# Performance work log

Measured on AMD Instinct MI355X. Metric: run time of the kernel, lower is better.

The kernel has to match this reference:

```python
import jax, jax.numpy as jnp
import numpy as np

GC = 32      # group_chans = dim // 4
DIM = 128
HEADS = 8
HD = 16      # head_dim
WS = 7       # window_size
EPS = 1e-5   # torch GroupNorm default eps


def setup_inputs() -> dict:
    key = jax.random.key(0)
    ks = jax.random.split(key, 16)
    f = lambda i, shape, s=0.1: jax.random.normal(ks[i], shape, jnp.float32) * s
    inp = {"x": jax.random.normal(ks[0], (2, 128, 56, 56, 56), jnp.float32)}
    kernels = [3, 5, 7, 9]
    names = ["loc", "s", "m", "l"]
    for j, (n, k) in enumerate(zip(names, kernels)):
        inp[f"w_{n}"] = f(1 + 2 * j, (GC, 1, k))   # depthwise conv weight
        inp[f"b_{n}"] = f(2 + 2 * j, (GC,))
    for n in ["d", "h", "w", "n"]:
        inp[f"g_{n}"] = jnp.ones((DIM,), jnp.float32)
        inp[f"bt_{n}"] = jnp.zeros((DIM,), jnp.float32)
    inp["wq"] = f(10, (DIM,))
    inp["wk"] = f(11, (DIM,))
    inp["wv"] = f(12, (DIM,))
    return inp


def dwconv1d(x, w, b):
    # x: (B, C, L), w: (C, 1, k) depthwise, SAME padding k//2
    k = w.shape[-1]
    y = jax.lax.conv_general_dilated(
        x, w, (1,), [(k // 2, k // 2)],
        dimension_numbers=("NCH", "OIH", "NCH"),
        feature_group_count=x.shape[1])
    return y + b[None, :, None]


def groupnorm(x, gamma, beta, groups):
    B, C = x.shape[0], x.shape[1]
    xg = x.reshape(B, groups, -1)
    mu = xg.mean(-1, keepdims=True)
    var = xg.var(-1, keepdims=True)
    xn = ((xg - mu) * jax.lax.rsqrt(var + EPS)).reshape(x.shape)
    bs = (1, C) + (1,) * (x.ndim - 2)
    return xn * gamma.reshape(bs) + beta.reshape(bs)


def axis_gate(s, w_loc, b_loc, w_s, b_s, w_m, b_m, w_l, b_l, g, bt):
    # s: (B, C, L) pooled signal; 4 depthwise conv branches over channel groups
    parts = [dwconv1d(s[:, i * GC:(i + 1) * GC], w, b)
             for i, (w, b) in enumerate([(w_loc, b_loc), (w_s, b_s), (w_m, b_m), (w_l, b_l)])]
    return jax.nn.sigmoid(groupnorm(jnp.concatenate(parts, axis=1), g, bt, 4))


def reference(x, w_loc, b_loc, w_s, b_s, w_m, b_m, w_l, b_l,
              g_d, bt_d, g_h, bt_h, g_w, bt_w, g_n, bt_n, wq, wk, wv):
    b, c, d, h, w = x.shape
    # axis-pooled signals
    x_d = x.mean(axis=(3, 4))  # (B,C,D)
    x_h = x.mean(axis=(2, 4))  # (B,C,H)
    x_w = x.mean(axis=(2, 3))  # (B,C,W)
    dw = (w_loc, b_loc, w_s, b_s, w_m, b_m, w_l, b_l)
    gd = axis_gate(x_d, *dw, g_d, bt_d)[:, :, :, None, None]
    gh = axis_gate(x_h, *dw, g_h, bt_h)[:, :, None, :, None]
    gw = axis_gate(x_w, *dw, g_w, bt_w)[:, :, None, None, :]
    xg = x * gd * gh * gw
    # avg-pool downsample by window_size
    dd, hh, ww = d // WS, h // WS, w // WS
    y = xg.reshape(b, c, dd, WS, hh, WS, ww, WS).mean(axis=(3, 5, 7))
    y = groupnorm(y, g_n, bt_n, 1)
    sh = (1, c, 1, 1, 1)
    # 1x1 grouped (depthwise) convs == per-channel scale, no bias
    q = (y * wq.reshape(sh)).reshape(b, HEADS, HD, -1)
    k = (y * wk.reshape(sh)).reshape(b, HEADS, HD, -1)
    v = (y * wv.reshape(sh)).reshape(b, HEADS, HD, -1)
    # channel-attention: (head_dim x head_dim) scores per head
    attn = jax.nn.softmax(jnp.einsum('bnis,bnjs->bnij', q, k) * (HD ** -0.5), axis=-1)
    o = jnp.einsum('bnij,bnjs->bnis', attn, v)      # (B, heads, hd, S)
    ca = jax.nn.sigmoid(o.mean(axis=-1).reshape(b, c, 1, 1, 1))
    return ca * xg
```

## Files before the change

### kernel.cpp

```cpp
#include <hip/hip_runtime.h>
#include <math.h>

#define B 2
#define C 128
#define DSZ 56
#define SL 3136
#define VOL 175616
#define S512 512
#define EPS 1e-5f

#define OFF_POOL 0
#define OFF_GATE 43008
#define OFF_Y    86016
#define OFF_STAT 217088
#define OFF_CA   217092
#define PCL 14336

__global__ __launch_bounds__(1024) void k1_pool(const float* __restrict__ x,
                                                float* __restrict__ ws) {
    int c = blockIdx.x, b = blockIdx.y;
    int bc = b * C + c;
    const float4* base = (const float4*)(x + (size_t)bc * VOL);
    int t = threadIdx.x;
    __shared__ float s_red[56 * 16];
    __shared__ float s_h[56];
    __shared__ float s_w[56];
    if (t < 56) { s_h[t] = 0.f; s_w[t] = 0.f; }
    bool active = (t < 784);
    int h = t / 14, w4 = t % 14;
    int lane = t & 63, wave = t >> 6;
    float hacc = 0.f, wa0 = 0.f, wa1 = 0.f, wa2 = 0.f, wa3 = 0.f;
    float4 v = active ? base[t] : make_float4(0.f, 0.f, 0.f, 0.f);
    for (int d = 0; d < 56; ++d) {
        float4 vn = make_float4(0.f, 0.f, 0.f, 0.f);
        if (d < 55 && active) vn = base[(d + 1) * 784 + t];
        float s4 = v.x + v.y + v.z + v.w;
        hacc += s4; wa0 += v.x; wa1 += v.y; wa2 += v.z; wa3 += v.w;
        float red = s4;
        #pragma unroll
        for (int off = 1; off < 64; off <<= 1) red += __shfl_xor(red, off);
        if (lane == 0) s_red[d * 16 + wave] = red;
        v = vn;
    }
    __syncthreads();
    if (active) {
        atomicAdd(&s_h[h], hacc);
        atomicAdd(&s_w[w4 * 4 + 0], wa0);
        atomicAdd(&s_w[w4 * 4 + 1], wa1);
        atomicAdd(&s_w[w4 * 4 + 2], wa2);
        atomicAdd(&s_w[w4 * 4 + 3], wa3);
    }
    __syncthreads();
    if (t < 56) {
        float dsum = 0.f;
        #pragma unroll
        for (int wv = 0; wv < 16; ++wv) dsum += s_red[t * 16 + wv];
        const float inv = 1.0f / 3136.0f;
        ws[OFF_POOL + 0 * PCL + bc * 56 + t] = dsum * inv;
        ws[OFF_POOL + 1 * PCL + bc * 56 + t] = s_h[t] * inv;
        ws[OFF_POOL + 2 * PCL + bc * 56 + t] = s_w[t] * inv;
    }
}

__global__ __launch_bounds__(256) void k2_gate(
    const float* __restrict__ w0, const float* __restrict__ b0,
    const float* __restrict__ w1, const float* __restrict__ b1,
    const float* __restrict__ w2, const float* __restrict__ b2,
    const float* __restrict__ w3, const float* __restrict__ b3,
    const float* __restrict__ g0, const float* __restrict__ be0,
    const float* __restrict__ g1, const float* __restrict__ be1,
    const float* __restrict__ g2, const float* __restrict__ be2,
    float* __restrict__ ws) {
    int idx = blockIdx.x;
    int sg = idx >> 3, rem = idx & 7;
    int b = rem >> 2, g = rem & 3;
    const float* wconv[4] = {w0, w1, w2, w3};
    const float* bconv[4] = {b0, b1, b2, b3};
    const float* gam[3] = {g0, g1, g2};
    const float* bet[3] = {be0, be1, be2};
    const int ksz[4] = {3, 5, 7, 9};
    int kg = ksz[g];
    int half = kg >> 1;
    __shared__ float s_in[32 * 56];
    __shared__ float s_wt[32 * 9];
    __shared__ float s_b[32];
    __shared__ float s_redu[8];
    int t = threadIdx.x;
    const float* sp = ws + OFF_POOL + sg * PCL + (b * C + g * 32) * 56;
    for (int e = t; e < 1792; e += 256) s_in[e] = sp[e];
    for (int e = t; e < 32 * kg; e += 256) s_wt[e] = wconv[g][e];
    if (t < 32) s_b[t] = bconv[g][t];
    __syncthreads();
    float vals[7];
    float sum = 0.f, sq = 0.f;
    {
        int ii = 0;
        for (int e = t; e < 1792; e += 256, ++ii) {
            int cl = e / 56, l = e % 56;
            float acc = s_b[cl];
            for (int tt = 0; tt < kg; ++tt) {
                int ll = l + tt - half;
                if (ll >= 0 && ll < 56) acc += s_in[cl * 56 + ll] * s_wt[cl * kg + tt];
            }
            vals[ii] = acc;
            sum += acc; sq += acc * acc;
        }
    }
    #pragma unroll
    for (int off = 1; off < 64; off <<= 1) {
        sum += __shfl_xor(sum, off);
        sq += __shfl_xor(sq, off);
    }
    int lane = t & 63, wv = t >> 6;
    if (lane == 0) { s_redu[wv] = sum; s_redu[4 + wv] = sq; }
    __syncthreads();
    sum = s_redu[0] + s_redu[1] + s_redu[2] + s_redu[3];
    sq = s_redu[4] + s_redu[5] + s_redu[6] + s_redu[7];
    float mean = sum / 1792.0f;
    float var = sq / 1792.0f - mean * mean;
    float rs = rsqrtf(var + EPS);
    float* gp = ws + OFF_GATE + sg * PCL + (b * C + g * 32) * 56;
    const float* ga = gam[sg];
    const float* be = bet[sg];
    {
        int ii = 0;
        for (int e = t; e < 1792; e += 256, ++ii) {
            int cl = e / 56;
            int cch = g * 32 + cl;
            float xn = (vals[ii] - mean) * rs * ga[cch] + be[cch];
            gp[e] = 1.0f / (1.0f + expf(-xn));
        }
    }
}

__global__ __launch_bounds__(256) void k3_pooly(const float* __restrict__ x,
                                                float* __restrict__ ws) {
    int dd = blockIdx.x, c = blockIdx.y, b = blockIdx.z;
    int bc = b * C + c;
    __shared__ float xs[SL];
    __shared__ float s_gh[56];
    __shared__ float s_gw[56];
    int t = threadIdx.x;
    const float* gp = ws + OFF_GATE;
    if (t < 56) s_gh[t] = gp[1 * PCL + bc * 56 + t];
    else if (t < 112) s_gw[t - 56] = gp[2 * PCL + bc * 56 + (t - 56)];
    float acc = 0.f;
    const float* xp = x + (size_t)bc * VOL + (size_t)dd * 7 * SL;
    int hh = (t & 63) >> 3, ww = t & 7;
    for (int dz = 0; dz < 7; ++dz) {
        __syncthreads();
        const float4* src = (const float4*)(xp + dz * SL);
        float4* dst = (float4*)xs;
        for (int e = t; e < 784; e += 256) dst[e] = src[e];
        __syncthreads();
        if (t < 64) {
            float part = 0.f;
            for (int r = 0; r < 7; ++r) {
                int h_ = hh * 7 + r;
                const float* row = &xs[h_ * 56 + ww * 7];
                float rsum = 0.f;
                #pragma unroll
                for (int q = 0; q < 7; ++q) rsum += row[q] * s_gw[ww * 7 + q];
                part += s_gh[h_] * rsum;
            }
            acc += part * gp[0 * PCL + bc * 56 + dd * 7 + dz];
        }
    }
    if (t < 64) ws[OFF_Y + bc * S512 + dd * 64 + t] = acc * (1.0f / 343.0f);
}

__global__ __launch_bounds__(256) void k4a_stats(float* __restrict__ ws) {
    int b = blockIdx.x;
    const float4* yp = (const float4*)(ws + OFF_Y + b * 65536);
    int t = threadIdx.x;
    float sum = 0.f, sq = 0.f;
    for (int e = t; e < 16384; e += 256) {
        float4 v = yp[e];
        sum += v.x + v.y + v.z + v.w;
        sq += v.x * v.x + v.y * v.y + v.z * v.z + v.w * v.w;
    }
    __shared__ float s_redu[8];
    #pragma unroll
    for (int off = 1; off < 64; off <<= 1) {
        sum += __shfl_xor(sum, off);
        sq += __shfl_xor(sq, off);
    }
    int lane = t & 63, wv = t >> 6;
    if (lane == 0) { s_redu[wv] = sum; s_redu[4 + wv] = sq; }
    __syncthreads();
    if (t == 0) {
        sum = s_redu[0] + s_redu[1] + s_redu[2] + s_redu[3];
        sq = s_redu[4] + s_redu[5] + s_redu[6] + s_redu[7];
        float mean = sum / 65536.0f;
        float var = sq / 65536.0f - mean * mean;
        ws[OFF_STAT + b * 2] = mean;
        ws[OFF_STAT + b * 2 + 1] = rsqrtf(var + EPS);
    }
}

__global__ __launch_bounds__(256) void k4b_attn(
    const float* __restrict__ gn, const float* __restrict__ btn,
    const float* __restrict__ wq, const float* __restrict__ wk,
    const float* __restrict__ wv, float* __restrict__ ws) {
    int blk = blockIdx.x;
    int b = blk >> 3, hd = blk & 7;
    __shared__ float yn[16 * 514];
    __shared__ float s_sc[256];
    __shared__ float s_ybar[16];
    int t = threadIdx.x;
    float mean = ws[OFF_STAT + b * 2];
    float rs = ws[OFF_STAT + b * 2 + 1];
    const float* yp = ws + OFF_Y + b * 65536 + hd * 16 * S512;
    for (int e = t; e < 8192; e += 256) {
        int i = e >> 9, s = e & 511;
        int cch = hd * 16 + i;
        yn[i * 514 + s] = (yp[e] - mean) * rs * gn[cch] + btn[cch];
    }
    __syncthreads();
    int i = t >> 4, j = t & 15;
    const float* ri = &yn[i * 514];
    const float* rj = &yn[j * 514];
    float g = 0.f;
    for (int s = 0; s < 512; ++s) g += ri[s] * rj[s];
    s_sc[t] = wq[hd * 16 + i] * wk[hd * 16 + j] * 0.25f * g;
    if (t < 16) {
        const float* r = &yn[t * 514];
        float sb = 0.f;
        for (int s = 0; s < 512; ++s) sb += r[s];
        s_ybar[t] = sb * (1.0f / 512.0f);
    }
    __syncthreads();
    if (t < 16) {
        float m = -1e30f;
        #pragma unroll
        for (int jj = 0; jj < 16; ++jj) m = fmaxf(m, s_sc[t * 16 + jj]);
        float den = 0.f, num = 0.f;
        #pragma unroll
        for (int jj = 0; jj < 16; ++jj) {
            float e = expf(s_sc[t * 16 + jj] - m);
            den += e;
            num += e * wv[hd * 16 + jj] * s_ybar[jj];
        }
        float o = num / den;
        ws[OFF_CA + b * C + hd * 16 + t] = 1.0f / (1.0f + expf(-o));
    }
}

__global__ __launch_bounds__(256) void k5_out(const float* __restrict__ x,
                                              const float* __restrict__ ws,
                                              float* __restrict__ out) {
    int d = blockIdx.x, c = blockIdx.y, b = blockIdx.z;
    int bc = b * C + c;
    __shared__ float s_gh[56];
    __shared__ float s_gw[56];
    int t = threadIdx.x;
    const float* gp = ws + OFF_GATE;
    if (t < 56) s_gh[t] = gp[1 * PCL + bc * 56 + t];
    else if (t < 112) s_gw[t - 56] = gp[2 * PCL + bc * 56 + (t - 56)];
    __syncthreads();
    float f = ws[OFF_CA + bc] * gp[0 * PCL + bc * 56 + d];
    const float4* xp = (const float4*)(x + (size_t)bc * VOL + (size_t)d * SL);
    float4* op = (float4*)(out + (size_t)bc * VOL + (size_t)d * SL);
    for (int e = t; e < 784; e += 256) {
        float4 v = xp[e];
        int o = e * 4;
        int h_ = o / 56;
        int w0 = o % 56;
        float fh = f * s_gh[h_];
        v.x *= fh * s_gw[w0];
        v.y *= fh * s_gw[w0 + 1];
        v.z *= fh * s_gw[w0 + 2];
        v.w *= fh * s_gw[w0 + 3];
        op[e] = v;
    }
}

extern "C" void kernel_launch(void* const* d_in, const int* in_sizes, int n_in,
                              void* d_out, int out_size, void* d_ws, size_t ws_size,
                              hipStream_t stream) {
    const float* x = (const float*)d_in[0];
    float* ws = (float*)d_ws;
    float* out = (float*)d_out;

    k1_pool<<<dim3(C, B), 1024, 0, stream>>>(x, ws);
    k2_gate<<<24, 256, 0, stream>>>(
        (const float*)d_in[1], (const float*)d_in[2],
        (const float*)d_in[3], (const float*)d_in[4],
        (const float*)d_in[5], (const float*)d_in[6],
        (const float*)d_in[7], (const float*)d_in[8],
        (const float*)d_in[9], (const float*)d_in[10],
        (const float*)d_in[11], (const float*)d_in[12],
        (const float*)d_in[13], (const float*)d_in[14],
        ws);
    k3_pooly<<<dim3(8, C, B), 256, 0, stream>>>(x, ws);
    k4a_stats<<<2, 256, 0, stream>>>(ws);
    k4b_attn<<<16, 256, 0, stream>>>(
        (const float*)d_in[15], (const float*)d_in[16],
        (const float*)d_in[17], (const float*)d_in[18],
        (const float*)d_in[19], ws);
    k5_out<<<dim3(56, C, B), 256, 0, stream>>>(x, ws, out);
}
```

Measured before the change: 443.3 us.

## Split pooling across depth slabs, widen stats reduction, vectorize attention and output

The first pooling kernel changes from one 1024-thread block per channel, which streamed all 56 depth slices, to 8 blocks per channel that each cover 7 depth slices. Partial H/W sums go to a new workspace area and a new combine kernel adds them up. The stats kernel moves to 1024 threads, the attention Gram loop reads float4 with padded rows, and the output kernel handles 4 depth slices per block with float4 W gates. The main aim is more parallelism for the memory-bound pooling pass, at the cost of an extra launch and extra workspace traffic.

```diff
diff --git a/kernel.cpp b/kernel.cpp
--- a/kernel.cpp
+++ b/kernel.cpp
@@ -3,63 +3,92 @@
 
 #define B 2
 #define C 128
-#define DSZ 56
 #define SL 3136
 #define VOL 175616
 #define S512 512
 #define EPS 1e-5f
+#define PCL 14336
 
 #define OFF_POOL 0
-#define OFF_GATE 43008
-#define OFF_Y    86016
-#define OFF_STAT 217088
-#define OFF_CA   217092
-#define PCL 14336
-
-__global__ __launch_bounds__(1024) void k1_pool(const float* __restrict__ x,
-                                                float* __restrict__ ws) {
-    int c = blockIdx.x, b = blockIdx.y;
+#define OFF_PPH  43008
+#define OFF_PPW  157696
+#define OFF_GATE 272384
+#define OFF_Y    315392
+#define OFF_STAT 446464
+#define OFF_CA   446468
+
+#define F4SUM(v) ((v).x + (v).y + (v).z + (v).w)
+
+__global__ __launch_bounds__(256) void k1_pool(const float* __restrict__ x,
+                                               float* __restrict__ ws) {
+    int dd = blockIdx.x, c = blockIdx.y, b = blockIdx.z;
     int bc = b * C + c;
-    const float4* base = (const float4*)(x + (size_t)bc * VOL);
-    int t = threadIdx.x;
-    __shared__ float s_red[56 * 16];
+    const float4* base = (const float4*)(x + (size_t)bc * VOL) + dd * 7 * 784;
+    int t = threadIdx.x;
+    int lane = t & 63, wave = t >> 6;
     __shared__ float s_h[56];
     __shared__ float s_w[56];
+    __shared__ float s_dred[7 * 4];
     if (t < 56) { s_h[t] = 0.f; s_w[t] = 0.f; }
-    bool active = (t < 784);
-    int h = t / 14, w4 = t % 14;
-    int lane = t & 63, wave = t >> 6;
-    float hacc = 0.f, wa0 = 0.f, wa1 = 0.f, wa2 = 0.f, wa3 = 0.f;
-    float4 v = active ? base[t] : make_float4(0.f, 0.f, 0.f, 0.f);
-    for (int d = 0; d < 56; ++d) {
-        float4 vn = make_float4(0.f, 0.f, 0.f, 0.f);
-        if (d < 55 && active) vn = base[(d + 1) * 784 + t];
-        float s4 = v.x + v.y + v.z + v.w;
-        hacc += s4; wa0 += v.x; wa1 += v.y; wa2 += v.z; wa3 += v.w;
-        float red = s4;
-        #pragma unroll
-        for (int off = 1; off < 64; off <<= 1) red += __shfl_xor(red, off);
-        if (lane == 0) s_red[d * 16 + wave] = red;
-        v = vn;
-    }
-    __syncthreads();
-    if (active) {
-        atomicAdd(&s_h[h], hacc);
-        atomicAdd(&s_w[w4 * 4 + 0], wa0);
-        atomicAdd(&s_w[w4 * 4 + 1], wa1);
-        atomicAdd(&s_w[w4 * 4 + 2], wa2);
-        atomicAdd(&s_w[w4 * 4 + 3], wa3);
-    }
-    __syncthreads();
+    __syncthreads();
+    float4 a0 = make_float4(0,0,0,0), a1 = make_float4(0,0,0,0);
+    float4 a2 = make_float4(0,0,0,0), a3 = make_float4(0,0,0,0);
+    #pragma unroll
+    for (int dz = 0; dz < 7; ++dz) {
+        const float4* sp = base + dz * 784;
+        float4 v0 = sp[t];
+        float4 v1 = sp[t + 256];
+        float4 v2 = sp[t + 512];
+        float4 v3 = make_float4(0,0,0,0);
+        if (t < 16) v3 = sp[t + 768];
+        a0.x += v0.x; a0.y += v0.y; a0.z += v0.z; a0.w += v0.w;
+        a1.x += v1.x; a1.y += v1.y; a1.z += v1.z; a1.w += v1.w;
+        a2.x += v2.x; a2.y += v2.y; a2.z += v2.z; a2.w += v2.w;
+        a3.x += v3.x; a3.y += v3.y; a3.z += v3.z; a3.w += v3.w;
+        float s4 = F4SUM(v0) + F4SUM(v1) + F4SUM(v2) + F4SUM(v3);
+        #pragma unroll
+        for (int off = 1; off < 64; off <<= 1) s4 += __shfl_xor(s4, off);
+        if (lane == 0) s_dred[dz * 4 + wave] = s4;
+    }
+    {
+        int s0 = t, s1 = t + 256, s2 = t + 512;
+        atomicAdd(&s_h[s0 / 14], F4SUM(a0));
+        atomicAdd(&s_h[s1 / 14], F4SUM(a1));
+        atomicAdd(&s_h[s2 / 14], F4SUM(a2));
+        int w0 = (s0 % 14) * 4, w1 = (s1 % 14) * 4, w2 = (s2 % 14) * 4;
+        atomicAdd(&s_w[w0 + 0], a0.x); atomicAdd(&s_w[w0 + 1], a0.y);
+        atomicAdd(&s_w[w0 + 2], a0.z); atomicAdd(&s_w[w0 + 3], a0.w);
+        atomicAdd(&s_w[w1 + 0], a1.x); atomicAdd(&s_w[w1 + 1], a1.y);
+        atomicAdd(&s_w[w1 + 2], a1.z); atomicAdd(&s_w[w1 + 3], a1.w);
+        atomicAdd(&s_w[w2 + 0], a2.x); atomicAdd(&s_w[w2 + 1], a2.y);
+        atomicAdd(&s_w[w2 + 2], a2.z); atomicAdd(&s_w[w2 + 3], a2.w);
+        if (t < 16) {
+            int s3 = t + 768, w3 = (s3 % 14) * 4;
+            atomicAdd(&s_h[s3 / 14], F4SUM(a3));
+            atomicAdd(&s_w[w3 + 0], a3.x); atomicAdd(&s_w[w3 + 1], a3.y);
+            atomicAdd(&s_w[w3 + 2], a3.z); atomicAdd(&s_w[w3 + 3], a3.w);
+        }
+    }
+    __syncthreads();
+    if (t < 7) {
+        float ds = s_dred[t * 4] + s_dred[t * 4 + 1] + s_dred[t * 4 + 2] + s_dred[t * 4 + 3];
+        ws[OFF_POOL + bc * 56 + dd * 7 + t] = ds * (1.0f / 3136.0f);
+    }
     if (t < 56) {
-        float dsum = 0.f;
-        #pragma unroll
-        for (int wv = 0; wv < 16; ++wv) dsum += s_red[t * 16 + wv];
-        const float inv = 1.0f / 3136.0f;
-        ws[OFF_POOL + 0 * PCL + bc * 56 + t] = dsum * inv;
-        ws[OFF_POOL + 1 * PCL + bc * 56 + t] = s_h[t] * inv;
-        ws[OFF_POOL + 2 * PCL + bc * 56 + t] = s_w[t] * inv;
-    }
+        ws[OFF_PPH + (bc * 8 + dd) * 56 + t] = s_h[t];
+        ws[OFF_PPW + (bc * 8 + dd) * 56 + t] = s_w[t];
+    }
+}
+
+__global__ __launch_bounds__(256) void k1b_combine(float* __restrict__ ws) {
+    int idx = blockIdx.x * 256 + threadIdx.x;
+    int axis = idx / 14336, rem = idx % 14336;
+    int bc = rem / 56, pos = rem % 56;
+    const float* p = ws + (axis ? OFF_PPW : OFF_PPH) + bc * 8 * 56 + pos;
+    float s = 0.f;
+    #pragma unroll
+    for (int dd = 0; dd < 8; ++dd) s += p[dd * 56];
+    ws[OFF_POOL + (1 + axis) * PCL + bc * 56 + pos] = s * (1.0f / 3136.0f);
 }
 
 __global__ __launch_bounds__(256) void k2_gate(
@@ -111,8 +140,8 @@
         sum += __shfl_xor(sum, off);
         sq += __shfl_xor(sq, off);
     }
-    int lane = t & 63, wv = t >> 6;
-    if (lane == 0) { s_redu[wv] = sum; s_redu[4 + wv] = sq; }
+    int lane = t & 63, wv_ = t >> 6;
+    if (lane == 0) { s_redu[wv_] = sum; s_redu[4 + wv_] = sq; }
     __syncthreads();
     sum = s_redu[0] + s_redu[1] + s_redu[2] + s_redu[3];
     sq = s_redu[4] + s_redu[5] + s_redu[6] + s_redu[7];
@@ -134,7 +163,7 @@
 }
 
 __global__ __launch_bounds__(256) void k3_pooly(const float* __restrict__ x,
-                                                float* __restrict__ ws) {
+                                               float* __restrict__ ws) {
     int dd = blockIdx.x, c = blockIdx.y, b = blockIdx.z;
     int bc = b * C + c;
     __shared__ float xs[SL];
@@ -169,28 +198,30 @@
     if (t < 64) ws[OFF_Y + bc * S512 + dd * 64 + t] = acc * (1.0f / 343.0f);
 }
 
-__global__ __launch_bounds__(256) void k4a_stats(float* __restrict__ ws) {
+__global__ __launch_bounds__(1024) void k4a_stats(float* __restrict__ ws) {
     int b = blockIdx.x;
     const float4* yp = (const float4*)(ws + OFF_Y + b * 65536);
     int t = threadIdx.x;
     float sum = 0.f, sq = 0.f;
-    for (int e = t; e < 16384; e += 256) {
-        float4 v = yp[e];
-        sum += v.x + v.y + v.z + v.w;
+    #pragma unroll
+    for (int k = 0; k < 16; ++k) {
+        float4 v = yp[t + k * 1024];
+        sum += F4SUM(v);
         sq += v.x * v.x + v.y * v.y + v.z * v.z + v.w * v.w;
     }
-    __shared__ float s_redu[8];
+    __shared__ float s_redu[32];
     #pragma unroll
     for (int off = 1; off < 64; off <<= 1) {
         sum += __shfl_xor(sum, off);
         sq += __shfl_xor(sq, off);
     }
-    int lane = t & 63, wv = t >> 6;
-    if (lane == 0) { s_redu[wv] = sum; s_redu[4 + wv] = sq; }
+    int lane = t & 63, wv_ = t >> 6;
+    if (lane == 0) { s_redu[wv_] = sum; s_redu[16 + wv_] = sq; }
     __syncthreads();
     if (t == 0) {
-        sum = s_redu[0] + s_redu[1] + s_redu[2] + s_redu[3];
-        sq = s_redu[4] + s_redu[5] + s_redu[6] + s_redu[7];
+        sum = 0.f; sq = 0.f;
+        #pragma unroll
+        for (int k = 0; k < 16; ++k) { sum += s_redu[k]; sq += s_redu[16 + k]; }
         float mean = sum / 65536.0f;
         float var = sq / 65536.0f - mean * mean;
         ws[OFF_STAT + b * 2] = mean;
@@ -204,30 +235,38 @@
     const float* __restrict__ wv, float* __restrict__ ws) {
     int blk = blockIdx.x;
     int b = blk >> 3, hd = blk & 7;
-    __shared__ float yn[16 * 514];
+    __shared__ float yn[16 * 516];
     __shared__ float s_sc[256];
     __shared__ float s_ybar[16];
     int t = threadIdx.x;
     float mean = ws[OFF_STAT + b * 2];
     float rs = ws[OFF_STAT + b * 2 + 1];
-    const float* yp = ws + OFF_Y + b * 65536 + hd * 16 * S512;
+    const float* yp = ws + OFF_Y + b * 65536 + hd * 8192;
     for (int e = t; e < 8192; e += 256) {
         int i = e >> 9, s = e & 511;
         int cch = hd * 16 + i;
-        yn[i * 514 + s] = (yp[e] - mean) * rs * gn[cch] + btn[cch];
+        yn[i * 516 + s] = (yp[e] - mean) * rs * gn[cch] + btn[cch];
     }
     __syncthreads();
     int i = t >> 4, j = t & 15;
-    const float* ri = &yn[i * 514];
-    const float* rj = &yn[j * 514];
+    const float4* ri = (const float4*)&yn[i * 516];
+    const float4* rj = (const float4*)&yn[j * 516];
     float g = 0.f;
-    for (int s = 0; s < 512; ++s) g += ri[s] * rj[s];
+    #pragma unroll 4
+    for (int s = 0; s < 128; ++s) {
+        float4 a = ri[s], c = rj[s];
+        g += a.x * c.x + a.y * c.y + a.z * c.z + a.w * c.w;
+    }
     s_sc[t] = wq[hd * 16 + i] * wk[hd * 16 + j] * 0.25f * g;
     if (t < 16) {
-        const float* r = &yn[t * 514];
-        float sb = 0.f;
-        for (int s = 0; s < 512; ++s) sb += r[s];
-        s_ybar[t] = sb * (1.0f / 512.0f);
+        const float4* r = (const float4*)&yn[t * 516];
+        float sx = 0.f, sy = 0.f, sz = 0.f, sw = 0.f;
+        #pragma unroll 4
+        for (int s = 0; s < 128; ++s) {
+            float4 a = r[s];
+            sx += a.x; sy += a.y; sz += a.z; sw += a.w;
+        }
+        s_ybar[t] = (sx + sy + sz + sw) * (1.0f / 512.0f);
     }
     __syncthreads();
     if (t < 16) {
@@ -249,29 +288,39 @@
 __global__ __launch_bounds__(256) void k5_out(const float* __restrict__ x,
                                               const float* __restrict__ ws,
                                               float* __restrict__ out) {
-    int d = blockIdx.x, c = blockIdx.y, b = blockIdx.z;
+    int d4 = blockIdx.x, c = blockIdx.y, b = blockIdx.z;
     int bc = b * C + c;
+    int t = threadIdx.x;
     __shared__ float s_gh[56];
-    __shared__ float s_gw[56];
-    int t = threadIdx.x;
+    __shared__ float4 s_gw4[14];
+    __shared__ float s_gd[4];
     const float* gp = ws + OFF_GATE;
     if (t < 56) s_gh[t] = gp[1 * PCL + bc * 56 + t];
-    else if (t < 112) s_gw[t - 56] = gp[2 * PCL + bc * 56 + (t - 56)];
-    __syncthreads();
-    float f = ws[OFF_CA + bc] * gp[0 * PCL + bc * 56 + d];
-    const float4* xp = (const float4*)(x + (size_t)bc * VOL + (size_t)d * SL);
-    float4* op = (float4*)(out + (size_t)bc * VOL + (size_t)d * SL);
-    for (int e = t; e < 784; e += 256) {
-        float4 v = xp[e];
-        int o = e * 4;
-        int h_ = o / 56;
-        int w0 = o % 56;
-        float fh = f * s_gh[h_];
-        v.x *= fh * s_gw[w0];
-        v.y *= fh * s_gw[w0 + 1];
-        v.z *= fh * s_gw[w0 + 2];
-        v.w *= fh * s_gw[w0 + 3];
-        op[e] = v;
+    else if (t < 70) s_gw4[t - 56] = ((const float4*)(gp + 2 * PCL + bc * 56))[t - 56];
+    else if (t < 74) s_gd[t - 70] = gp[0 * PCL + bc * 56 + d4 * 4 + (t - 70)] * ws[OFF_CA + bc];
+    __syncthreads();
+    const float4* xp = (const float4*)(x + (size_t)bc * VOL) + d4 * 4 * 784;
+    float4* op = (float4*)(out + (size_t)bc * VOL) + d4 * 4 * 784;
+    #pragma unroll
+    for (int i = 0; i < 4; ++i) {
+        float gd = s_gd[i];
+        #pragma unroll
+        for (int k = 0; k < 3; ++k) {
+            int e = t + k * 256;
+            float4 v = xp[i * 784 + e];
+            float fh = gd * s_gh[e / 14];
+            float4 gw = s_gw4[e % 14];
+            v.x *= fh * gw.x; v.y *= fh * gw.y; v.z *= fh * gw.z; v.w *= fh * gw.w;
+            op[i * 784 + e] = v;
+        }
+        if (t < 16) {
+            int e = t + 768;
+            float4 v = xp[i * 784 + e];
+            float fh = gd * s_gh[e / 14];
+            float4 gw = s_gw4[e % 14];
+            v.x *= fh * gw.x; v.y *= fh * gw.y; v.z *= fh * gw.z; v.w *= fh * gw.w;
+            op[i * 784 + e] = v;
+        }
     }
 }
 
@@ -282,7 +331,8 @@
     float* ws = (float*)d_ws;
     float* out = (float*)d_out;
 
-    k1_pool<<<dim3(C, B), 1024, 0, stream>>>(x, ws);
+    k1_pool<<<dim3(8, C, B), 256, 0, stream>>>(x, ws);
+    k1b_combine<<<112, 256, 0, stream>>>(ws);
     k2_gate<<<24, 256, 0, stream>>>(
         (const float*)d_in[1], (const float*)d_in[2],
         (const float*)d_in[3], (const float*)d_in[4],
@@ -293,10 +343,10 @@
         (const float*)d_in[13], (const float*)d_in[14],
         ws);
     k3_pooly<<<dim3(8, C, B), 256, 0, stream>>>(x, ws);
-    k4a_stats<<<2, 256, 0, stream>>>(ws);
+    k4a_stats<<<2, 1024, 0, stream>>>(ws);
     k4b_attn<<<16, 256, 0, stream>>>(
         (const float*)d_in[15], (const float*)d_in[16],
         (const float*)d_in[17], (const float*)d_in[18],
         (const float*)d_in[19], ws);
-    k5_out<<<dim3(56, C, B), 256, 0, stream>>>(x, ws, out);
-}
+    k5_out<<<dim3(14, C, B), 256, 0, stream>>>(x, ws, out);
+}
```

New measurement: 457.2 us. 3.2% more time.
